# Kernel tuning notes

Measured on AMD Instinct MI355X. Metric: run time of the kernel, lower is better.

## Reference

```python
import jax, jax.numpy as jnp
import numpy as np

H = 4          # number of heads
C = 32         # head dim (H*C == D)
INF = 1e9
EPS = 1e-5


def setup_inputs() -> dict:
    key = jax.random.key(0)
    ks = jax.random.split(key, 8)
    B, N, D = 1, 256, 128
    x = jax.random.normal(ks[0], (B, N, N, D), dtype=jnp.float32)
    mask = jnp.ones((B, N, N), dtype=jnp.float32)
    s = 1.0 / np.sqrt(D)
    return {
        "x": x,
        "mask": mask,
        "ln_w": jnp.ones((D,), jnp.float32),
        "ln_b": jnp.zeros((D,), jnp.float32),
        "w_tri": jax.random.normal(ks[1], (D, H), jnp.float32) * s,
        "w_q": jax.random.normal(ks[2], (D, H * C), jnp.float32) * s,
        "w_k": jax.random.normal(ks[3], (D, H * C), jnp.float32) * s,
        "w_v": jax.random.normal(ks[4], (D, H * C), jnp.float32) * s,
        "w_g": jax.random.normal(ks[5], (D, H * C), jnp.float32) * s,
        "b_g": jnp.ones((H * C,), jnp.float32),
        "w_o": jax.random.normal(ks[6], (H * C, D), jnp.float32) * s,
        "b_o": jnp.zeros((D,), jnp.float32),
    }


def reference(x, mask, ln_w, ln_b, w_tri, w_q, w_k, w_v, w_g, b_g, w_o, b_o):
    B, I, J, D = x.shape
    # LayerNorm over channel dim
    mu = jnp.mean(x, axis=-1, keepdims=True)
    var = jnp.mean(jnp.square(x - mu), axis=-1, keepdims=True)
    xn = (x - mu) * jax.lax.rsqrt(var + EPS) * ln_w + ln_b

    # Triangle bias: linear D->H, permute_final_dims((2,0,1)) -> [B,H,I,J], unsqueeze(-4) -> [B,1,H,I,J]
    tri_bias = jnp.einsum("bijd,dh->bhij", xn, w_tri)[:, None]
    # Mask bias: inf*(mask[...,:,None,None,:]-1) -> [B,I,1,1,J]
    mask_bias = INF * (mask[:, :, None, None, :] - 1.0)

    # Gated MHA per row I, attending across columns J
    q = (xn @ w_q).reshape(B, I, J, H, C) * (1.0 / np.sqrt(C))
    k = (xn @ w_k).reshape(B, I, J, H, C)
    v = (xn @ w_v).reshape(B, I, J, H, C)
    scores = jnp.einsum("bimhc,binhc->bihmn", q, k) + tri_bias + mask_bias
    attn = jax.nn.softmax(scores, axis=-1)
    o = jnp.einsum("bihmn,binhc->bimhc", attn, v)
    g = jax.nn.sigmoid((xn @ w_g + b_g).reshape(B, I, J, H, C))
    o = (g * o).reshape(B, I, J, H * C)
    return o @ w_o + b_o
```

## Files before the change

### kernel.cpp

```cpp
#include <hip/hip_runtime.h>
#include <hip/hip_bf16.h>

#define INF_F 1e9f
#define EPS_F 1e-5f
#define QSCALE 0.1767766952966369f
#define SM_SHIFT 16.0f
#define LOG2E 1.44269504088896340736f

typedef __attribute__((ext_vector_type(8))) short short8;
typedef __attribute__((ext_vector_type(4))) short bf16x4;
typedef __attribute__((ext_vector_type(4))) float f32x4;

__device__ __forceinline__ unsigned short f2bf(float f) {
    union { float f; unsigned int u; } v; v.f = f;
    return (unsigned short)((v.u + 0x8000u) >> 16);
}
__device__ __forceinline__ float bf2f(unsigned short b) {
    union { unsigned int u; float f; } v; v.u = ((unsigned int)b) << 16; return v.f;
}
__device__ __forceinline__ unsigned int pack2bf(float a, float b) {
    union { float f; unsigned int u; } ua, ub; ua.f = a; ub.f = b;
    return __builtin_amdgcn_perm(ub.u + 0x8000u, ua.u + 0x8000u, 0x07060302u);
}

#if defined(__has_builtin)
#if __has_builtin(__builtin_amdgcn_mfma_f32_16x16x16bf16_1k)
#define MFMA16BF(a, b, c) __builtin_amdgcn_mfma_f32_16x16x16bf16_1k(a, b, c, 0, 0, 0)
#endif
#endif
#ifndef MFMA16BF
__device__ __forceinline__ f32x4 mfma16bf_asm(bf16x4 a, bf16x4 b, f32x4 c) {
    asm volatile("v_mfma_f32_16x16x16_bf16 %0, %1, %2, %0\n\ts_nop 7\n\ts_nop 7"
                 : "+v"(c) : "v"(a), "v"(b));
    return c;
}
#define MFMA16BF(a, b, c) mfma16bf_asm(a, b, c)
#endif

__global__ __launch_bounds__(256) void prep_weights(
    const float* __restrict__ wq, const float* __restrict__ wk,
    const float* __restrict__ wv, const float* __restrict__ wg,
    const float* __restrict__ wo, unsigned short* __restrict__ wt)
{
    const int m = blockIdx.x;
    const float* W = (m == 0) ? wq : (m == 1) ? wk : (m == 2) ? wv : (m == 3) ? wg : wo;
    const float scale = (m == 0) ? QSCALE * LOG2E : 1.0f;
    unsigned short* out = wt + m * 16384;
    const int t = threadIdx.x;
    #pragma unroll
    for (int j = 0; j < 8; ++j) {
        int o = t * 64 + j * 8;
        int n = o >> 7, k0 = o & 127;
        short8 v;
        #pragma unroll
        for (int jj = 0; jj < 8; ++jj)
            v[jj] = (short)f2bf(W[(size_t)(k0 + jj) * 128 + n] * scale);
        *reinterpret_cast<short8*>(out + o) = v;
    }
}

__global__ __launch_bounds__(256) void ln_proj_kernel(
    const float* __restrict__ x, const float* __restrict__ ln_w, const float* __restrict__ ln_b,
    const float* __restrict__ w_tri, const unsigned short* __restrict__ wt,
    const float* __restrict__ b_g,
    unsigned short* __restrict__ qb, unsigned short* __restrict__ kb,
    unsigned short* __restrict__ vb, unsigned short* __restrict__ gb,
    float* __restrict__ tri_bias)
{
    __shared__ unsigned short As[64][136];
    __shared__ unsigned short Bs[128][136];
    __shared__ float wt_s[512];
    __shared__ float bgs[128];

    const int tid = threadIdx.x;
    const int p0  = blockIdx.x * 64;

    if (tid < 128) bgs[tid] = b_g[tid];
    wt_s[tid] = w_tri[tid];
    wt_s[tid + 256] = w_tri[tid + 256];

    {
        const int c4 = (tid & 31) * 4;
        const float4 lw = *reinterpret_cast<const float4*>(ln_w + c4);
        const float4 lb = *reinterpret_cast<const float4*>(ln_b + c4);
        #pragma unroll
        for (int r = 0; r < 8; ++r) {
            int idx = r * 256 + tid;
            int px  = idx >> 5;
            float4 v = *reinterpret_cast<const float4*>(x + (size_t)(p0 + px) * 128 + c4);
            float s  = v.x + v.y + v.z + v.w;
            float ss = v.x * v.x + v.y * v.y + v.z * v.z + v.w * v.w;
            #pragma unroll
            for (int mk = 1; mk <= 16; mk <<= 1) {
                s  += __shfl_xor(s, mk);
                ss += __shfl_xor(ss, mk);
            }
            float mu   = s * 0.0078125f;
            float rstd = rsqrtf(ss * 0.0078125f - mu * mu + EPS_F);
            float a0 = (v.x - mu) * rstd * lw.x + lb.x;
            float a1 = (v.y - mu) * rstd * lw.y + lb.y;
            float a2 = (v.z - mu) * rstd * lw.z + lb.z;
            float a3 = (v.w - mu) * rstd * lw.w + lb.w;
            *reinterpret_cast<unsigned int*>(&As[px][c4])     = pack2bf(a0, a1);
            *reinterpret_cast<unsigned int*>(&As[px][c4 + 2]) = pack2bf(a2, a3);
        }
    }
    __syncthreads();

    {
        const int px = tid >> 2, hh = tid & 3;
        float acc = 0.f;
        #pragma unroll
        for (int kq = 0; kq < 128; kq += 8) {
            short8 xv = *reinterpret_cast<const short8*>(&As[px][kq]);
            #pragma unroll
            for (int j = 0; j < 8; ++j)
                acc = fmaf(bf2f((unsigned short)xv[j]), wt_s[(kq + j) * 4 + hh], acc);
        }
        tri_bias[hh * 65536 + p0 + px] = (acc - SM_SHIFT) * LOG2E;
    }

    const int lane = tid & 63, wid = tid >> 6;
    const int lrow = lane & 15, lgrp = lane >> 4;
    const int m0 = wid * 16;

    for (int y = 0; y < 4; ++y) {
        __syncthreads();
        const unsigned short* W = wt + y * 16384;
        #pragma unroll
        for (int r = 0; r < 8; ++r) {
            int idx = r * 256 + tid;
            int n = idx >> 4, k8 = (idx & 15) * 8;
            *reinterpret_cast<short8*>(&Bs[n][k8]) =
                *reinterpret_cast<const short8*>(W + n * 128 + k8);
        }
        __syncthreads();

        f32x4 acc[8];
        #pragma unroll
        for (int nt = 0; nt < 8; ++nt) acc[nt] = f32x4{0.f, 0.f, 0.f, 0.f};
        #pragma unroll
        for (int kk = 0; kk < 4; ++kk) {
            short8 af = *reinterpret_cast<const short8*>(&As[m0 + lrow][kk * 32 + lgrp * 8]);
            short8 bfr[8];
            #pragma unroll
            for (int nt = 0; nt < 8; ++nt)
                bfr[nt] = *reinterpret_cast<const short8*>(&Bs[nt * 16 + lrow][kk * 32 + lgrp * 8]);
            #pragma unroll
            for (int nt = 0; nt < 8; ++nt)
                acc[nt] = __builtin_amdgcn_mfma_f32_16x16x32_bf16(af, bfr[nt], acc[nt], 0, 0, 0);
        }
        __syncthreads();

        #pragma unroll
        for (int nt = 0; nt < 8; ++nt)
            #pragma unroll
            for (int r = 0; r < 4; ++r) {
                int row = m0 + lgrp * 4 + r;
                int col = nt * 16 + lrow;
                float vv = acc[nt][r];
                if (y == 3) vv = 1.f / (1.f + __expf(-(vv + bgs[col])));
                Bs[row][col] = f2bf(vv);
            }
        __syncthreads();

        unsigned short* outp = (y == 0) ? qb : (y == 1) ? kb : (y == 2) ? vb : gb;
        #pragma unroll
        for (int r = 0; r < 4; ++r) {
            int idx = r * 256 + tid;
            int px = idx >> 4, c8 = (idx & 15) * 8;
            *reinterpret_cast<short8*>(outp + (size_t)(p0 + px) * 128 + c8) =
                *reinterpret_cast<const short8*>(&Bs[px][c8]);
        }
    }
}

__global__ __launch_bounds__(512) void attn_kernel(
    const unsigned short* qbuf, const unsigned short* __restrict__ kbuf,
    const unsigned short* __restrict__ vbuf, const unsigned short* __restrict__ gbuf,
    const float* __restrict__ tri_bias, const float* __restrict__ mask,
    unsigned short* og)
{
    __shared__ unsigned short Ks[256][40];
    __shared__ unsigned short Vt[32][264];
    __shared__ float maskb[256];

    const int tid = threadIdx.x;
    const int i  = blockIdx.x;
    const int h  = blockIdx.y >> 1;
    const int rg = blockIdx.y & 1;
    const size_t base = (size_t)i * 32768 + (size_t)h * 32;

    #pragma unroll
    for (int r = 0; r < 2; ++r) {
        int idx = r * 512 + tid;
        int n = idx >> 2, c8 = (idx & 3) * 8;
        short8 kv = *reinterpret_cast<const short8*>(kbuf + base + (size_t)n * 128 + c8);
        short8 vv = *reinterpret_cast<const short8*>(vbuf + base + (size_t)n * 128 + c8);
        *reinterpret_cast<short8*>(&Ks[n][c8]) = kv;
        #pragma unroll
        for (int j = 0; j < 8; ++j) {
            int row = c8 + j;
            Vt[row][n ^ (((row >> 3) & 3) << 4)] = (unsigned short)vv[j];
        }
    }
    if (tid < 256) maskb[tid] = (INF_F * LOG2E) * (mask[i * 256 + tid] - 1.0f);
    __syncthreads();

    const int lane = tid & 63;
    const int wid  = tid >> 6;
    const int q    = lane & 15;
    const int g    = lane >> 4;
    const int q0   = rg * 128 + wid * 16;

    short8 qf = *reinterpret_cast<const short8*>(qbuf + base + (size_t)(q0 + q) * 128 + g * 8);

    const float* biasrow = tri_bias + (size_t)h * 65536 + (size_t)(q0 + q) * 256;
    const f32x4 z = {0.f, 0.f, 0.f, 0.f};
    f32x4 oacc[2] = {z, z};
    float lsum = 0.f;
    const int xr0 = ((q >> 3) & 1) << 4;
    const int xr1 = ((2 + (q >> 3)) & 3) << 4;

    short8 kfa = *reinterpret_cast<const short8*>(&Ks[q][g * 8]);
    short8 kfb = *reinterpret_cast<const short8*>(&Ks[16 + q][g * 8]);
    f32x4 ca = *reinterpret_cast<const f32x4*>(biasrow + g * 4)
             + *reinterpret_cast<const f32x4*>(&maskb[g * 4]);
    f32x4 cb = *reinterpret_cast<const f32x4*>(biasrow + 16 + g * 4)
             + *reinterpret_cast<const f32x4*>(&maskb[16 + g * 4]);
    bf16x4 vA0 = *reinterpret_cast<const bf16x4*>(&Vt[q][(g * 4) ^ xr0]);
    bf16x4 vA1 = *reinterpret_cast<const bf16x4*>(&Vt[16 + q][(g * 4) ^ xr1]);
    bf16x4 vB0 = *reinterpret_cast<const bf16x4*>(&Vt[q][(16 + g * 4) ^ xr0]);
    bf16x4 vB1 = *reinterpret_cast<const bf16x4*>(&Vt[16 + q][(16 + g * 4) ^ xr1]);

    #pragma unroll
    for (int ch = 0; ch < 8; ++ch) {
        short8 kfa_n, kfb_n; f32x4 ca_n, cb_n;
        bf16x4 vA0_n, vA1_n, vB0_n, vB1_n;
        if (ch < 7) {
            const int nbn = (ch + 1) * 32;
            kfa_n = *reinterpret_cast<const short8*>(&Ks[nbn + q][g * 8]);
            kfb_n = *reinterpret_cast<const short8*>(&Ks[nbn + 16 + q][g * 8]);
            ca_n = *reinterpret_cast<const f32x4*>(biasrow + nbn + g * 4)
                 + *reinterpret_cast<const f32x4*>(&maskb[nbn + g * 4]);
            cb_n = *reinterpret_cast<const f32x4*>(biasrow + nbn + 16 + g * 4)
                 + *reinterpret_cast<const f32x4*>(&maskb[nbn + 16 + g * 4]);
            vA0_n = *reinterpret_cast<const bf16x4*>(&Vt[q][(nbn + g * 4) ^ xr0]);
            vA1_n = *reinterpret_cast<const bf16x4*>(&Vt[16 + q][(nbn + g * 4) ^ xr1]);
            vB0_n = *reinterpret_cast<const bf16x4*>(&Vt[q][(nbn + 16 + g * 4) ^ xr0]);
            vB1_n = *reinterpret_cast<const bf16x4*>(&Vt[16 + q][(nbn + 16 + g * 4) ^ xr1]);
        }
        f32x4 s0 = __builtin_amdgcn_mfma_f32_16x16x32_bf16(kfa, qf, ca, 0, 0, 0);
        f32x4 s1 = __builtin_amdgcn_mfma_f32_16x16x32_bf16(kfb, qf, cb, 0, 0, 0);
        float p00 = exp2f(s0[0]), p01 = exp2f(s0[1]);
        float p02 = exp2f(s0[2]), p03 = exp2f(s0[3]);
        float p10 = exp2f(s1[0]), p11 = exp2f(s1[1]);
        float p12 = exp2f(s1[2]), p13 = exp2f(s1[3]);
        lsum += ((p00 + p01) + (p02 + p03)) + ((p10 + p11) + (p12 + p13));
        union { unsigned int u[2]; bf16x4 s; } pA, pB;
        pA.u[0] = pack2bf(p00, p01); pA.u[1] = pack2bf(p02, p03);
        pB.u[0] = pack2bf(p10, p11); pB.u[1] = pack2bf(p12, p13);
        oacc[0] = MFMA16BF(pA.s, vA0, oacc[0]);
        oacc[1] = MFMA16BF(pA.s, vA1, oacc[1]);
        oacc[0] = MFMA16BF(pB.s, vB0, oacc[0]);
        oacc[1] = MFMA16BF(pB.s, vB1, oacc[1]);
        kfa = kfa_n; kfb = kfb_n; ca = ca_n; cb = cb_n;
        vA0 = vA0_n; vA1 = vA1_n; vB0 = vB0_n; vB1 = vB1_n;
    }

    lsum += __shfl_xor(lsum, 16);
    lsum += __shfl_xor(lsum, 32);

    float linv = 1.0f / lsum;
    #pragma unroll
    for (int r = 0; r < 4; ++r) {
        float li = __shfl(linv, g * 4 + r);
        int m = q0 + g * 4 + r;
        #pragma unroll
        for (int ct = 0; ct < 2; ++ct) {
            int c = ct * 16 + q;
            float gv = bf2f(gbuf[base + (size_t)m * 128 + c]);
            og[base + (size_t)m * 128 + c] = f2bf(oacc[ct][r] * li * gv);
        }
    }
}

__global__ __launch_bounds__(256) void out_proj_kernel(
    const unsigned short* __restrict__ og, const unsigned short* __restrict__ wto,
    const float* __restrict__ b_o, float* __restrict__ out)
{
    __shared__ unsigned short As[64][136];
    __shared__ unsigned short Bs[128][136];
    __shared__ float bos[128];

    const int tid = threadIdx.x;
    const int p0  = blockIdx.x * 64;
    if (tid < 128) bos[tid] = b_o[tid];

    #pragma unroll
    for (int r = 0; r < 4; ++r) {
        int idx = r * 256 + tid;
        int px = idx >> 4, k8 = (idx & 15) * 8;
        *reinterpret_cast<short8*>(&As[px][k8]) =
            *reinterpret_cast<const short8*>(og + (size_t)(p0 + px) * 128 + k8);
    }
    #pragma unroll
    for (int r = 0; r < 8; ++r) {
        int idx = r * 256 + tid;
        int n = idx >> 4, k8 = (idx & 15) * 8;
        *reinterpret_cast<short8*>(&Bs[n][k8]) =
            *reinterpret_cast<const short8*>(wto + n * 128 + k8);
    }
    __syncthreads();

    const int lane = tid & 63, wid = tid >> 6;
    const int lrow = lane & 15, lgrp = lane >> 4;
    const int m0 = wid * 16;

    f32x4 acc[8];
    #pragma unroll
    for (int nt = 0; nt < 8; ++nt) acc[nt] = f32x4{0.f, 0.f, 0.f, 0.f};

    #pragma unroll
    for (int kk = 0; kk < 4; ++kk) {
        short8 af = *reinterpret_cast<const short8*>(&As[m0 + lrow][kk * 32 + lgrp * 8]);
        short8 bfr[8];
        #pragma unroll
        for (int nt = 0; nt < 8; ++nt)
            bfr[nt] = *reinterpret_cast<const short8*>(&Bs[nt * 16 + lrow][kk * 32 + lgrp * 8]);
        #pragma unroll
        for (int nt = 0; nt < 8; ++nt)
            acc[nt] = __builtin_amdgcn_mfma_f32_16x16x32_bf16(af, bfr[nt], acc[nt], 0, 0, 0);
    }

    #pragma unroll
    for (int nt = 0; nt < 8; ++nt)
        #pragma unroll
        for (int r = 0; r < 4; ++r) {
            int row = m0 + lgrp * 4 + r;
            int col = nt * 16 + lrow;
            out[(size_t)(p0 + row) * 128 + col] = acc[nt][r] + bos[col];
        }
}

extern "C" void kernel_launch(void* const* d_in, const int* in_sizes, int n_in,
                              void* d_out, int out_size, void* d_ws, size_t ws_size,
                              hipStream_t stream)
{
    const float* x     = (const float*)d_in[0];
    const float* mask  = (const float*)d_in[1];
    const float* ln_w  = (const float*)d_in[2];
    const float* ln_b  = (const float*)d_in[3];
    const float* w_tri = (const float*)d_in[4];
    const float* w_q   = (const float*)d_in[5];
    const float* w_k   = (const float*)d_in[6];
    const float* w_v   = (const float*)d_in[7];
    const float* w_g   = (const float*)d_in[8];
    const float* b_g   = (const float*)d_in[9];
    const float* w_o   = (const float*)d_in[10];
    const float* b_o   = (const float*)d_in[11];
    float* out = (float*)d_out;

    unsigned short* qb = (unsigned short*)d_ws;
    unsigned short* kb = qb + 8388608;
    unsigned short* vb = kb + 8388608;
    unsigned short* gb = vb + 8388608;
    float* bias = (float*)(gb + 8388608);
    unsigned short* wt = (unsigned short*)(bias + 4 * 65536);

    prep_weights<<<dim3(5), 256, 0, stream>>>(w_q, w_k, w_v, w_g, w_o, wt);
    ln_proj_kernel<<<1024, 256, 0, stream>>>(
        x, ln_w, ln_b, w_tri, wt, b_g, qb, kb, vb, gb, bias);
    attn_kernel<<<dim3(256, 8), 512, 0, stream>>>(
        qb, kb, vb, gb, bias, mask, qb );
    out_proj_kernel<<<1024, 256, 0, stream>>>(qb, wt + 4 * 16384, b_o, out);
}
```

Before: 103.3 us.

## Double rows per block in LN-projection and read weight fragments directly from global

The LN+projection kernel now handles 128 pixels per block instead of 64 and launches half as many blocks. Each wave computes two 16-row MFMA tiles that share the same weight fragments. Those fragments are now loaded straight from global (L2-cached) memory instead of being staged through a shared-memory B tile, which removes several barriers per projection. Results are written directly to global as scattered 2-byte stores rather than through a shared-memory transpose, which trades coalesced 16-byte stores for fewer syncs and less LDS.

```diff
diff --git a/kernel.cpp b/kernel.cpp
--- a/kernel.cpp
+++ b/kernel.cpp
@@ -67,13 +67,12 @@
     unsigned short* __restrict__ vb, unsigned short* __restrict__ gb,
     float* __restrict__ tri_bias)
 {
-    __shared__ unsigned short As[64][136];
-    __shared__ unsigned short Bs[128][136];
+    __shared__ unsigned short As[128][136];
     __shared__ float wt_s[512];
     __shared__ float bgs[128];
 
     const int tid = threadIdx.x;
-    const int p0  = blockIdx.x * 64;
+    const int p0  = blockIdx.x * 128;
 
     if (tid < 128) bgs[tid] = b_g[tid];
     wt_s[tid] = w_tri[tid];
@@ -84,7 +83,7 @@
         const float4 lw = *reinterpret_cast<const float4*>(ln_w + c4);
         const float4 lb = *reinterpret_cast<const float4*>(ln_b + c4);
         #pragma unroll
-        for (int r = 0; r < 8; ++r) {
+        for (int r = 0; r < 16; ++r) {
             int idx = r * 256 + tid;
             int px  = idx >> 5;
             float4 v = *reinterpret_cast<const float4*>(x + (size_t)(p0 + px) * 128 + c4);
@@ -107,8 +106,10 @@
     }
     __syncthreads();
 
-    {
-        const int px = tid >> 2, hh = tid & 3;
+    #pragma unroll
+    for (int r = 0; r < 2; ++r) {
+        int idx = r * 256 + tid;
+        int px = idx >> 2, hh = idx & 3;
         float acc = 0.f;
         #pragma unroll
         for (int kq = 0; kq < 128; kq += 8) {
@@ -122,56 +123,46 @@
 
     const int lane = tid & 63, wid = tid >> 6;
     const int lrow = lane & 15, lgrp = lane >> 4;
-    const int m0 = wid * 16;
+    const int m0 = wid * 32;
 
     for (int y = 0; y < 4; ++y) {
-        __syncthreads();
         const unsigned short* W = wt + y * 16384;
-        #pragma unroll
-        for (int r = 0; r < 8; ++r) {
-            int idx = r * 256 + tid;
-            int n = idx >> 4, k8 = (idx & 15) * 8;
-            *reinterpret_cast<short8*>(&Bs[n][k8]) =
-                *reinterpret_cast<const short8*>(W + n * 128 + k8);
-        }
-        __syncthreads();
-
-        f32x4 acc[8];
-        #pragma unroll
-        for (int nt = 0; nt < 8; ++nt) acc[nt] = f32x4{0.f, 0.f, 0.f, 0.f};
+        f32x4 acc[2][8];
+        #pragma unroll
+        for (int mt = 0; mt < 2; ++mt)
+            #pragma unroll
+            for (int nt = 0; nt < 8; ++nt) acc[mt][nt] = f32x4{0.f, 0.f, 0.f, 0.f};
+
         #pragma unroll
         for (int kk = 0; kk < 4; ++kk) {
-            short8 af = *reinterpret_cast<const short8*>(&As[m0 + lrow][kk * 32 + lgrp * 8]);
-            short8 bfr[8];
+            short8 wf[8];
             #pragma unroll
             for (int nt = 0; nt < 8; ++nt)
-                bfr[nt] = *reinterpret_cast<const short8*>(&Bs[nt * 16 + lrow][kk * 32 + lgrp * 8]);
-            #pragma unroll
-            for (int nt = 0; nt < 8; ++nt)
-                acc[nt] = __builtin_amdgcn_mfma_f32_16x16x32_bf16(af, bfr[nt], acc[nt], 0, 0, 0);
-        }
-        __syncthreads();
-
-        #pragma unroll
-        for (int nt = 0; nt < 8; ++nt)
-            #pragma unroll
-            for (int r = 0; r < 4; ++r) {
-                int row = m0 + lgrp * 4 + r;
+                wf[nt] = *reinterpret_cast<const short8*>(
+                    W + (nt * 16 + lrow) * 128 + kk * 32 + lgrp * 8);
+            short8 af0 = *reinterpret_cast<const short8*>(&As[m0 + lrow][kk * 32 + lgrp * 8]);
+            short8 af1 = *reinterpret_cast<const short8*>(&As[m0 + 16 + lrow][kk * 32 + lgrp * 8]);
+            #pragma unroll
+            for (int nt = 0; nt < 8; ++nt) {
+                acc[0][nt] = __builtin_amdgcn_mfma_f32_16x16x32_bf16(af0, wf[nt], acc[0][nt], 0, 0, 0);
+                acc[1][nt] = __builtin_amdgcn_mfma_f32_16x16x32_bf16(af1, wf[nt], acc[1][nt], 0, 0, 0);
+            }
+        }
+
+        unsigned short* outp = (y == 0) ? qb : (y == 1) ? kb : (y == 2) ? vb : gb;
+        #pragma unroll
+        for (int mt = 0; mt < 2; ++mt)
+            #pragma unroll
+            for (int nt = 0; nt < 8; ++nt) {
                 int col = nt * 16 + lrow;
-                float vv = acc[nt][r];
-                if (y == 3) vv = 1.f / (1.f + __expf(-(vv + bgs[col])));
-                Bs[row][col] = f2bf(vv);
+                #pragma unroll
+                for (int r = 0; r < 4; ++r) {
+                    int row = m0 + mt * 16 + lgrp * 4 + r;
+                    float vv = acc[mt][nt][r];
+                    if (y == 3) vv = 1.f / (1.f + __expf(-(vv + bgs[col])));
+                    outp[(size_t)(p0 + row) * 128 + col] = f2bf(vv);
+                }
             }
-        __syncthreads();
-
-        unsigned short* outp = (y == 0) ? qb : (y == 1) ? kb : (y == 2) ? vb : gb;
-        #pragma unroll
-        for (int r = 0; r < 4; ++r) {
-            int idx = r * 256 + tid;
-            int px = idx >> 4, c8 = (idx & 15) * 8;
-            *reinterpret_cast<short8*>(outp + (size_t)(p0 + px) * 128 + c8) =
-                *reinterpret_cast<const short8*>(&Bs[px][c8]);
-        }
     }
 }
 
@@ -369,7 +360,7 @@
     unsigned short* wt = (unsigned short*)(bias + 4 * 65536);
 
     prep_weights<<<dim3(5), 256, 0, stream>>>(w_q, w_k, w_v, w_g, w_o, wt);
-    ln_proj_kernel<<<1024, 256, 0, stream>>>(
+    ln_proj_kernel<<<512, 256, 0, stream>>>(
         x, ln_w, ln_b, w_tri, wt, b_g, qb, kb, vb, gb, bias);
     attn_kernel<<<dim3(256, 8), 512, 0, stream>>>(
         qb, kb, vb, gb, bias, mask, qb );
```

Measured after the change: 122.9 us. 19.0% more time.

## Enlarge LN-projection tiles, prefetch weights in registers, store outputs directly

Applied to the files above, without the earlier changes.

The LayerNorm+projection kernel now uses 512-thread blocks covering 128 pixels, with the A and B shared tiles aliased into one buffer. The activation fragments are held in registers for the whole kernel. The next projection's weights are prefetched into registers while the current MFMA loop runs, which removes one barrier and the global-to-shared stall per projection. Results are written straight from the accumulators to global memory as 2-byte stores rather than staged through shared memory for 16-byte coalesced stores. That trade risks less efficient global writes.

```diff
diff --git a/kernel.cpp b/kernel.cpp
--- a/kernel.cpp
+++ b/kernel.cpp
@@ -59,7 +59,7 @@
     }
 }
 
-__global__ __launch_bounds__(256) void ln_proj_kernel(
+__global__ __launch_bounds__(512, 4) void ln_proj_kernel(
     const float* __restrict__ x, const float* __restrict__ ln_w, const float* __restrict__ ln_b,
     const float* __restrict__ w_tri, const unsigned short* __restrict__ wt,
     const float* __restrict__ b_g,
@@ -67,17 +67,17 @@
     unsigned short* __restrict__ vb, unsigned short* __restrict__ gb,
     float* __restrict__ tri_bias)
 {
-    __shared__ unsigned short As[64][136];
-    __shared__ unsigned short Bs[128][136];
+    __shared__ unsigned short smem[128 * 136];
     __shared__ float wt_s[512];
     __shared__ float bgs[128];
+    unsigned short (*As)[136] = reinterpret_cast<unsigned short(*)[136]>(smem);
+    unsigned short (*Bs)[136] = reinterpret_cast<unsigned short(*)[136]>(smem);
 
     const int tid = threadIdx.x;
-    const int p0  = blockIdx.x * 64;
+    const int p0  = blockIdx.x * 128;
 
     if (tid < 128) bgs[tid] = b_g[tid];
-    wt_s[tid] = w_tri[tid];
-    wt_s[tid + 256] = w_tri[tid + 256];
+    if (tid < 512) wt_s[tid] = w_tri[tid & 511];
 
     {
         const int c4 = (tid & 31) * 4;
@@ -85,7 +85,7 @@
         const float4 lb = *reinterpret_cast<const float4*>(ln_b + c4);
         #pragma unroll
         for (int r = 0; r < 8; ++r) {
-            int idx = r * 256 + tid;
+            int idx = r * 512 + tid;
             int px  = idx >> 5;
             float4 v = *reinterpret_cast<const float4*>(x + (size_t)(p0 + px) * 128 + c4);
             float s  = v.x + v.y + v.z + v.w;
@@ -124,54 +124,60 @@
     const int lrow = lane & 15, lgrp = lane >> 4;
     const int m0 = wid * 16;
 
+    short8 af[4];
+    #pragma unroll
+    for (int kk = 0; kk < 4; ++kk)
+        af[kk] = *reinterpret_cast<const short8*>(&As[m0 + lrow][kk * 32 + lgrp * 8]);
+
+    short8 wreg[4];
+    #pragma unroll
+    for (int p = 0; p < 4; ++p)
+        wreg[p] = *reinterpret_cast<const short8*>(wt + (p * 512 + tid) * 8);
+
+    __syncthreads();
+
     for (int y = 0; y < 4; ++y) {
+        #pragma unroll
+        for (int p = 0; p < 4; ++p) {
+            int idx = p * 512 + tid;
+            *reinterpret_cast<short8*>(&Bs[idx >> 4][(idx & 15) * 8]) = wreg[p];
+        }
         __syncthreads();
-        const unsigned short* W = wt + y * 16384;
-        #pragma unroll
-        for (int r = 0; r < 8; ++r) {
-            int idx = r * 256 + tid;
-            int n = idx >> 4, k8 = (idx & 15) * 8;
-            *reinterpret_cast<short8*>(&Bs[n][k8]) =
-                *reinterpret_cast<const short8*>(W + n * 128 + k8);
-        }
-        __syncthreads();
+
+        if (y < 3) {
+            const unsigned short* Wn = wt + (y + 1) * 16384;
+            #pragma unroll
+            for (int p = 0; p < 4; ++p)
+                wreg[p] = *reinterpret_cast<const short8*>(Wn + (p * 512 + tid) * 8);
+        }
 
         f32x4 acc[8];
         #pragma unroll
         for (int nt = 0; nt < 8; ++nt) acc[nt] = f32x4{0.f, 0.f, 0.f, 0.f};
         #pragma unroll
         for (int kk = 0; kk < 4; ++kk) {
-            short8 af = *reinterpret_cast<const short8*>(&As[m0 + lrow][kk * 32 + lgrp * 8]);
-            short8 bfr[8];
+            short8 wf[8];
             #pragma unroll
             for (int nt = 0; nt < 8; ++nt)
-                bfr[nt] = *reinterpret_cast<const short8*>(&Bs[nt * 16 + lrow][kk * 32 + lgrp * 8]);
+                wf[nt] = *reinterpret_cast<const short8*>(&Bs[nt * 16 + lrow][kk * 32 + lgrp * 8]);
             #pragma unroll
             for (int nt = 0; nt < 8; ++nt)
-                acc[nt] = __builtin_amdgcn_mfma_f32_16x16x32_bf16(af, bfr[nt], acc[nt], 0, 0, 0);
-        }
-        __syncthreads();
-
-        #pragma unroll
-        for (int nt = 0; nt < 8; ++nt)
+                acc[nt] = __builtin_amdgcn_mfma_f32_16x16x32_bf16(af[kk], wf[nt], acc[nt], 0, 0, 0);
+        }
+
+        unsigned short* outp = (y == 0) ? qb : (y == 1) ? kb : (y == 2) ? vb : gb;
+        #pragma unroll
+        for (int nt = 0; nt < 8; ++nt) {
+            int col = nt * 16 + lrow;
             #pragma unroll
             for (int r = 0; r < 4; ++r) {
                 int row = m0 + lgrp * 4 + r;
-                int col = nt * 16 + lrow;
                 float vv = acc[nt][r];
                 if (y == 3) vv = 1.f / (1.f + __expf(-(vv + bgs[col])));
-                Bs[row][col] = f2bf(vv);
+                outp[(size_t)(p0 + row) * 128 + col] = f2bf(vv);
             }
+        }
         __syncthreads();
-
-        unsigned short* outp = (y == 0) ? qb : (y == 1) ? kb : (y == 2) ? vb : gb;
-        #pragma unroll
-        for (int r = 0; r < 4; ++r) {
-            int idx = r * 256 + tid;
-            int px = idx >> 4, c8 = (idx & 15) * 8;
-            *reinterpret_cast<short8*>(outp + (size_t)(p0 + px) * 128 + c8) =
-                *reinterpret_cast<const short8*>(&Bs[px][c8]);
-        }
     }
 }
 
@@ -369,7 +375,7 @@
     unsigned short* wt = (unsigned short*)(bias + 4 * 65536);
 
     prep_weights<<<dim3(5), 256, 0, stream>>>(w_q, w_k, w_v, w_g, w_o, wt);
-    ln_proj_kernel<<<1024, 256, 0, stream>>>(
+    ln_proj_kernel<<<512, 512, 0, stream>>>(
         x, ln_w, ln_b, w_tri, wt, b_g, qb, kb, vb, gb, bias);
     attn_kernel<<<dim3(256, 8), 512, 0, stream>>>(
         qb, kb, vb, gb, bias, mask, qb );
```

Result: faster. 96.05 us (-7.0%).
